# Kernel optimization log

Hardware: AMD Instinct MI355X
Metric: run time of the kernel (lower is better)

## Reference

```python
import jax, jax.numpy as jnp
import numpy as np

N = 50000
IN_F = 512
HID = 64
HEADS = 4
CLASSES = 6
E = 800000
NEG_SLOPE = 0.2


def setup_inputs() -> dict:
    key = jax.random.key(0)
    ks = jax.random.split(key, 12)
    s = 1.0 / np.sqrt(IN_F)
    s2 = 1.0 / np.sqrt(HID * HEADS)
    return {
        "x": jax.random.normal(ks[0], (N, IN_F), dtype=jnp.float32),
        "edge_index": jax.random.randint(ks[1], (2, E), 0, N, dtype=jnp.int32),
        "W1": jax.random.normal(ks[2], (IN_F, HEADS * HID), dtype=jnp.float32) * s,
        "a_src1": jax.random.normal(ks[3], (HEADS, HID), dtype=jnp.float32) * s,
        "a_dst1": jax.random.normal(ks[4], (HEADS, HID), dtype=jnp.float32) * s,
        "b1": jnp.zeros((HEADS * HID,), dtype=jnp.float32),
        "W2": jax.random.normal(ks[5], (HEADS * HID, CLASSES), dtype=jnp.float32) * s2,
        "a_src2": jax.random.normal(ks[6], (1, CLASSES), dtype=jnp.float32) * s2,
        "a_dst2": jax.random.normal(ks[7], (1, CLASSES), dtype=jnp.float32) * s2,
        "b2": jnp.zeros((CLASSES,), dtype=jnp.float32),
    }


def gat_conv(x, src, dst, W, a_src, a_dst, bias, heads, ch):
    # x: [N, F] -> h: [N, H, C]
    n = x.shape[0]
    h = (x @ W).reshape(n, heads, ch)
    # per-node attention halves: [N, H]
    e_src = jnp.einsum('nhc,hc->nh', h, a_src)
    e_dst = jnp.einsum('nhc,hc->nh', h, a_dst)
    # per-edge logits with leaky relu: [E', H]
    logits = jax.nn.leaky_relu(e_src[src] + e_dst[dst], NEG_SLOPE)
    # segment softmax over incoming edges of each dst node
    m = jax.ops.segment_max(logits, dst, num_segments=n)  # [N, H]
    p = jnp.exp(logits - m[dst])
    denom = jax.ops.segment_sum(p, dst, num_segments=n)   # [N, H] (>0: self loops)
    alpha = p / denom[dst]                                 # [E', H]
    # weighted scatter-aggregate: [N, H, C]
    out = jax.ops.segment_sum(alpha[:, :, None] * h[src], dst, num_segments=n)
    return out.reshape(n, heads * ch) + bias


def reference(x, edge_index, W1, a_src1, a_dst1, b1, W2, a_src2, a_dst2, b2):
    n = x.shape[0]
    loops = jnp.arange(n, dtype=edge_index.dtype)
    src = jnp.concatenate([edge_index[0], loops])  # PyG add_self_loops
    dst = jnp.concatenate([edge_index[1], loops])
    h = gat_conv(x, src, dst, W1, a_src1, a_dst1, b1, HEADS, HID)
    h = jax.nn.elu(h)
    out = gat_conv(h, src, dst, W2, a_src2, a_dst2, b2, 1, CLASSES)
    return jax.nn.log_softmax(out, axis=1)
```

## Files before the change

kernel.cpp:

```cpp
#include <hip/hip_runtime.h>

#define HEADS 4
#define HID 64
#define CH1 256
#define CLS 6
#define H2S 8
#define NSLOPE 0.2f

typedef short bf16x8 __attribute__((ext_vector_type(8)));
typedef float f32x4 __attribute__((ext_vector_type(4)));

__device__ __forceinline__ float leaky(float x) {
  return (x >= 0.f) ? x : NSLOPE * x;
}

__device__ __forceinline__ ushort f2bf(float f) {
  unsigned u = __float_as_uint(f);
  unsigned r = (u + 0x7FFFu + ((u >> 16) & 1u)) >> 16;
  return (ushort)r;
}

__device__ __forceinline__ float bf2f(ushort u) {
  return __uint_as_float((unsigned)u << 16);
}

__device__ __forceinline__ void gload16(const void* g, void* l) {
  __builtin_amdgcn_global_load_lds((const __attribute__((address_space(1))) void*)g,
                                   (__attribute__((address_space(3))) void*)l, 16, 0, 0);
}

__global__ void k_count_cvt_x(const int* __restrict__ ei, int E, int Etot,
                              int* __restrict__ cnt, int eb,
                              const float* __restrict__ W1, ushort* __restrict__ w1t,
                              const float* __restrict__ x, ushort* __restrict__ xb,
                              long nx) {
  int b = blockIdx.x;
  if (b < eb) {
    int e = b * 256 + threadIdx.x;
    if (e >= Etot) return;
    int d = (e < E) ? ei[E + e] : e - E;
    atomicAdd(&cnt[d], 1);
  } else if (b < eb + 512) {
    int t = (b - eb) * 256 + threadIdx.x;
    if (t >= 512 * 256) return;
    int k = t >> 8, c = t & 255;
    w1t[c * 512 + k] = f2bf(W1[t]);
  } else {
    long i = ((long)(b - eb - 512) * 256 + threadIdx.x) * 4;
    long stride = 2048L * 1024;
    for (; i + 3 < nx; i += stride) {
      float4 v = *(const float4*)&x[i];
      ushort4 o;
      o.x = f2bf(v.x); o.y = f2bf(v.y); o.z = f2bf(v.z); o.w = f2bf(v.w);
      *(ushort4*)&xb[i] = o;
    }
  }
}

__global__ __launch_bounds__(256) void k_gemm1_scatter(
    const ushort* __restrict__ xb,
    const ushort* __restrict__ w1t,
    const float* __restrict__ a_src, const float* __restrict__ a_dst,
    ushort* __restrict__ h1b, float* __restrict__ es, float* __restrict__ ed,
    int M, int G1,
    const int* __restrict__ ei, int E, int Etot,
    const int* __restrict__ rowptr, int* __restrict__ cursor,
    int* __restrict__ esrc) {
  __shared__ ushort lds[2][10240];
  int t = threadIdx.x;

  if (blockIdx.x >= G1) {
    int e = (blockIdx.x - G1) * 256 + t;
    if (e >= Etot) return;
    int s, d;
    if (e < E) { s = ei[e]; d = ei[E + e]; } else { s = d = e - E; }
    int pos = rowptr[d] + atomicAdd(&cursor[d], 1);
    esrc[pos] = s;
    return;
  }

  int wid = t >> 6, lane = t & 63;
  int brow = blockIdx.x * 64;

  int rA = t >> 2;
  int sA = (t & 3) ^ (rA & 3);
  int rowA = brow + rA; if (rowA >= M) rowA = M - 1;
  const ushort* srcA  = xb  + (size_t)rowA * 512 + sA * 8;
  int cB = t >> 2;
  int sB = (t & 3) ^ (cB & 3);
  const ushort* srcB0 = w1t + (size_t)cB * 512 + sB * 8;
  int dA = t * 8;
  int dB = 2048 + t * 8;

  int l15 = lane & 15, g = lane >> 4;
  int sw = ((g ^ (lane & 3)) << 3);
  int aoff[4], boff[4];
#pragma unroll
  for (int m = 0; m < 4; ++m) aoff[m] = (m * 16 + l15) * 32 + sw;
#pragma unroll
  for (int n = 0; n < 4; ++n) boff[n] = 2048 + (wid * 64 + n * 16 + l15) * 32 + sw;

  f32x4 acc[4][4] = {};

#define STAGE(buf, koff) do { \
    gload16(srcA + (koff),              &lds[buf][dA]); \
    gload16(srcB0 + (koff),             &lds[buf][dB]); \
    gload16(srcB0 +  64 * 512 + (koff), &lds[buf][dB + 2048]); \
    gload16(srcB0 + 128 * 512 + (koff), &lds[buf][dB + 4096]); \
    gload16(srcB0 + 192 * 512 + (koff), &lds[buf][dB + 6144]); \
  } while (0)

  STAGE(0, 0);
  __syncthreads();
  int cur = 0;
  for (int kt = 0; kt < 16; ++kt) {
    if (kt < 15) STAGE(cur ^ 1, (kt + 1) * 32);
    const ushort* L = lds[cur];
    bf16x8 av[4], bv[4];
#pragma unroll
    for (int m = 0; m < 4; ++m) av[m] = *(const bf16x8*)&L[aoff[m]];
#pragma unroll
    for (int n = 0; n < 4; ++n) bv[n] = *(const bf16x8*)&L[boff[n]];
#pragma unroll
    for (int m = 0; m < 4; ++m)
#pragma unroll
      for (int n = 0; n < 4; ++n)
        acc[m][n] = __builtin_amdgcn_mfma_f32_16x16x32_bf16(av[m], bv[n], acc[m][n], 0, 0, 0);
    __syncthreads();
    cur ^= 1;
  }
#undef STAGE

  float as4[4], ad4[4];
#pragma unroll
  for (int n = 0; n < 4; ++n) {
    int c = wid * 64 + n * 16 + l15;
    as4[n] = a_src[c];
    ad4[n] = a_dst[c];
  }
  int rbase = g * 4;
#pragma unroll
  for (int m = 0; m < 4; ++m) {
#pragma unroll
    for (int r = 0; r < 4; ++r) {
      int grow = brow + m * 16 + rbase + r;
      bool ok = grow < M;
      float ps = 0.f, pd = 0.f;
#pragma unroll
      for (int n = 0; n < 4; ++n) {
        float v = acc[m][n][r];
        ps += v * as4[n];
        pd += v * ad4[n];
        if (ok) h1b[(size_t)grow * CH1 + wid * 64 + n * 16 + l15] = f2bf(v);
      }
#pragma unroll
      for (int o = 1; o < 16; o <<= 1) {
        ps += __shfl_xor(ps, o);
        pd += __shfl_xor(pd, o);
      }
      if (l15 == 0 && ok) {
        es[grow * HEADS + wid] = ps;
        ed[grow * HEADS + wid] = pd;
      }
    }
  }
}

__global__ __launch_bounds__(256) void k_scan1(int* __restrict__ deg,
    int* __restrict__ rowptr, int* __restrict__ bsum, int n) {
  int i = blockIdx.x * 256 + threadIdx.x;
  int v = (i < n) ? deg[i] : 0;
  if (i < n) deg[i] = 0;
  int lane = threadIdx.x & 63, wave = threadIdx.x >> 6;
  int incl = v;
#pragma unroll
  for (int o = 1; o < 64; o <<= 1) {
    int u = __shfl_up(incl, o);
    if (lane >= o) incl += u;
  }
  __shared__ int ws4[4];
  if (lane == 63) ws4[wave] = incl;
  __syncthreads();
  if (threadIdx.x == 0) {
    int run = 0;
    for (int w = 0; w < 4; ++w) { int x = ws4[w]; ws4[w] = run; run += x; }
    bsum[blockIdx.x] = run;
  }
  __syncthreads();
  if (i < n) rowptr[i] = incl - v + ws4[wave];
}

__global__ __launch_bounds__(256) void k_scan3(int* __restrict__ rowptr,
    const int* __restrict__ bsum, int n, int Etot, int nb) {
  int t = threadIdx.x;
  int b = blockIdx.x;
  int v = (t < b && t < nb) ? bsum[t] : 0;
  int lane = t & 63, wave = t >> 6;
#pragma unroll
  for (int o = 32; o; o >>= 1) v += __shfl_xor(v, o);
  __shared__ int ws4[4];
  if (lane == 0) ws4[wave] = v;
  __syncthreads();
  int base = ws4[0] + ws4[1] + ws4[2] + ws4[3];
  int i = b * 256 + t;
  if (i < n) rowptr[i] += base;
  if (i == 0) rowptr[n] = Etot;
}

__global__ __launch_bounds__(256) void k_agg1_csr(const int* __restrict__ rowptr,
    const int* __restrict__ esrc, const float* __restrict__ es,
    const float* __restrict__ ed, const ushort* __restrict__ h1b,
    const float* __restrict__ b1, const float* __restrict__ W2,
    const float* __restrict__ a_src2, const float* __restrict__ a_dst2,
    float* __restrict__ h2, float* __restrict__ es2, float* __restrict__ ed2,
    int Nn) {
  __shared__ int   spi[4][64];
  __shared__ float spp[4][64 * 4];
  int wid = threadIdx.x >> 6, lane = threadIdx.x & 63;
  int ch = lane * 4;
  float w2s[4][CLS];
#pragma unroll
  for (int c = 0; c < 4; ++c)
#pragma unroll
    for (int j = 0; j < CLS; ++j)
      w2s[c][j] = W2[(ch + c) * CLS + j];

  int d = blockIdx.x * 4 + wid;
  if (d >= Nn) return;
  int beg = rowptr[d], end = rowptr[d + 1];
  float4 edv = *(const float4*)&ed[d * 4];
  int myhead = lane >> 4;
  const char* hcb = (const char*)h1b + (size_t)ch * 2;

  float4 acc = make_float4(0.f, 0.f, 0.f, 0.f);
  float4 den4 = make_float4(0.f, 0.f, 0.f, 0.f);
  const float* pp = &spp[wid][0];
  for (int c0 = beg; c0 < end; c0 += 64) {
    int i = c0 + lane;
    int s = 0;
    float4 p = make_float4(0.f, 0.f, 0.f, 0.f);
    if (i < end) {
      s = esrc[i];
      float4 e4 = *(const float4*)&es[s * 4];
      p.x = __expf(leaky(e4.x + edv.x));
      p.y = __expf(leaky(e4.y + edv.y));
      p.z = __expf(leaky(e4.z + edv.z));
      p.w = __expf(leaky(e4.w + edv.w));
    }
    den4.x += p.x; den4.y += p.y; den4.z += p.z; den4.w += p.w;
    spi[wid][lane] = s << 9;
    *(float4*)&spp[wid][lane * 4] = p;
    int cl = min(64, end - c0);
    int j = 0;
    for (; j + 3 < cl; j += 4) {
      int o0 = spi[wid][j],     o1 = spi[wid][j + 1];
      int o2 = spi[wid][j + 2], o3 = spi[wid][j + 3];
      float p0 = pp[j * 4 + myhead],       p1 = pp[(j + 1) * 4 + myhead];
      float p2 = pp[(j + 2) * 4 + myhead], p3 = pp[(j + 3) * 4 + myhead];
      ushort4 v0 = *(const ushort4*)(hcb + o0);
      ushort4 v1 = *(const ushort4*)(hcb + o1);
      ushort4 v2 = *(const ushort4*)(hcb + o2);
      ushort4 v3 = *(const ushort4*)(hcb + o3);
      acc.x += p0 * bf2f(v0.x) + p1 * bf2f(v1.x) + p2 * bf2f(v2.x) + p3 * bf2f(v3.x);
      acc.y += p0 * bf2f(v0.y) + p1 * bf2f(v1.y) + p2 * bf2f(v2.y) + p3 * bf2f(v3.y);
      acc.z += p0 * bf2f(v0.z) + p1 * bf2f(v1.z) + p2 * bf2f(v2.z) + p3 * bf2f(v3.z);
      acc.w += p0 * bf2f(v0.w) + p1 * bf2f(v1.w) + p2 * bf2f(v2.w) + p3 * bf2f(v3.w);
    }
    for (; j < cl; ++j) {
      int oj = spi[wid][j];
      float pj = pp[j * 4 + myhead];
      ushort4 v = *(const ushort4*)(hcb + oj);
      acc.x += pj * bf2f(v.x);
      acc.y += pj * bf2f(v.y);
      acc.z += pj * bf2f(v.z);
      acc.w += pj * bf2f(v.w);
    }
  }
#pragma unroll
  for (int o = 32; o; o >>= 1) {
    den4.x += __shfl_xor(den4.x, o);
    den4.y += __shfl_xor(den4.y, o);
    den4.z += __shfl_xor(den4.z, o);
    den4.w += __shfl_xor(den4.w, o);
  }
  float den = (myhead == 0) ? den4.x : (myhead == 1) ? den4.y
            : (myhead == 2) ? den4.z : den4.w;
  float4 b4 = *(const float4*)&b1[ch];
  float4 r;
  r.x = acc.x / den + b4.x; r.x = (r.x > 0.f) ? r.x : expm1f(r.x);
  r.y = acc.y / den + b4.y; r.y = (r.y > 0.f) ? r.y : expm1f(r.y);
  r.z = acc.z / den + b4.z; r.z = (r.z > 0.f) ? r.z : expm1f(r.z);
  r.w = acc.w / den + b4.w; r.w = (r.w > 0.f) ? r.w : expm1f(r.w);

  float q0 = r.x * w2s[0][0] + r.y * w2s[1][0] + r.z * w2s[2][0] + r.w * w2s[3][0];
  float q1 = r.x * w2s[0][1] + r.y * w2s[1][1] + r.z * w2s[2][1] + r.w * w2s[3][1];
  float q2 = r.x * w2s[0][2] + r.y * w2s[1][2] + r.z * w2s[2][2] + r.w * w2s[3][2];
  float q3 = r.x * w2s[0][3] + r.y * w2s[1][3] + r.z * w2s[2][3] + r.w * w2s[3][3];
  float q4 = r.x * w2s[0][4] + r.y * w2s[1][4] + r.z * w2s[2][4] + r.w * w2s[3][4];
  float q5 = r.x * w2s[0][5] + r.y * w2s[1][5] + r.z * w2s[2][5] + r.w * w2s[3][5];
#pragma unroll
  for (int o = 32; o; o >>= 1) {
    q0 += __shfl_xor(q0, o); q1 += __shfl_xor(q1, o); q2 += __shfl_xor(q2, o);
    q3 += __shfl_xor(q3, o); q4 += __shfl_xor(q4, o); q5 += __shfl_xor(q5, o);
  }
  if (lane == 0) {
    float* h2r = &h2[(size_t)d * H2S];
    h2r[0] = q0; h2r[1] = q1; h2r[2] = q2; h2r[3] = q3; h2r[4] = q4; h2r[5] = q5;
    es2[d] = q0 * a_src2[0] + q1 * a_src2[1] + q2 * a_src2[2]
           + q3 * a_src2[3] + q4 * a_src2[4] + q5 * a_src2[5];
    ed2[d] = q0 * a_dst2[0] + q1 * a_dst2[1] + q2 * a_dst2[2]
           + q3 * a_dst2[3] + q4 * a_dst2[4] + q5 * a_dst2[5];
  }
}

__global__ __launch_bounds__(256) void k_l2(const int* __restrict__ rowptr,
    const int* __restrict__ esrc, const float* __restrict__ es2,
    const float* __restrict__ ed2, const float* __restrict__ h2,
    const float* __restrict__ b2, float* __restrict__ out, int Nn) {
  int t = threadIdx.x;
  int grp = t >> 3, sl = t & 7;
  int n = blockIdx.x * 32 + grp;
  if (n >= Nn) return;
  int beg = rowptr[n], end = rowptr[n + 1];
  float edv = ed2[n];
  float den = 0.f, a0 = 0.f, a1 = 0.f, a2 = 0.f, a3 = 0.f, a4 = 0.f, a5 = 0.f;
  for (int i = beg + sl; i < end; i += 8) {
    int s = esrc[i];
    float p = __expf(leaky(es2[s] + edv));
    den += p;
    const float* hr = &h2[(size_t)s * H2S];
    float4 v0 = *(const float4*)hr;
    float2 v1 = *(const float2*)(hr + 4);
    a0 += p * v0.x; a1 += p * v0.y; a2 += p * v0.z;
    a3 += p * v0.w; a4 += p * v1.x; a5 += p * v1.y;
  }
#pragma unroll
  for (int o = 1; o < 8; o <<= 1) {
    den += __shfl_xor(den, o);
    a0 += __shfl_xor(a0, o); a1 += __shfl_xor(a1, o); a2 += __shfl_xor(a2, o);
    a3 += __shfl_xor(a3, o); a4 += __shfl_xor(a4, o); a5 += __shfl_xor(a5, o);
  }
  if (sl == 0) {
    float v[CLS];
    v[0] = a0 / den + b2[0]; v[1] = a1 / den + b2[1]; v[2] = a2 / den + b2[2];
    v[3] = a3 / den + b2[3]; v[4] = a4 / den + b2[4]; v[5] = a5 / den + b2[5];
    float mx = -1e30f;
#pragma unroll
    for (int j = 0; j < CLS; ++j) mx = fmaxf(mx, v[j]);
    float sum = 0.f;
#pragma unroll
    for (int j = 0; j < CLS; ++j) sum += __expf(v[j] - mx);
    float l = mx + logf(sum);
#pragma unroll
    for (int j = 0; j < CLS; ++j) out[n * CLS + j] = v[j] - l;
  }
}

extern "C" void kernel_launch(void* const* d_in, const int* in_sizes, int n_in,
                              void* d_out, int out_size, void* d_ws, size_t ws_size,
                              hipStream_t stream) {
  const float* x      = (const float*)d_in[0];
  const int*   ei     = (const int*)d_in[1];
  const float* W1     = (const float*)d_in[2];
  const float* a_src1 = (const float*)d_in[3];
  const float* a_dst1 = (const float*)d_in[4];
  const float* b1     = (const float*)d_in[5];
  const float* W2     = (const float*)d_in[6];
  const float* a_src2 = (const float*)d_in[7];
  const float* a_dst2 = (const float*)d_in[8];
  const float* b2     = (const float*)d_in[9];
  float* out = (float*)d_out;

  const int IN_F = 512;
  int N = in_sizes[0] / IN_F;
  int E = in_sizes[1] / 2;
  int Etot = E + N;

  float* ws = (float*)d_ws;
  size_t off = 0;
  ushort* xb  = (ushort*)(ws + off); off += (size_t)N * 256;
  ushort* h1b = (ushort*)(ws + off); off += (size_t)N * 128;
  float* es1  = ws + off; off += (size_t)N * HEADS;
  float* ed1  = ws + off; off += (size_t)N * HEADS;
  float* h2   = ws + off; off += (size_t)N * H2S;
  float* es2  = ws + off; off += (size_t)N;
  float* ed2  = ws + off; off += (size_t)N;
  int* rowptr = (int*)(ws + off); off += (size_t)N + 1;
  int* cursor = (int*)(ws + off); off += (size_t)N;
  int* bsum   = (int*)(ws + off); off += 256;
  int* esrc   = (int*)(ws + off); off += (size_t)Etot;
  ushort* w1t = (ushort*)(ws + off); off += (512 * 256 * 2 + 3) / 4;

  int nb = (N + 255) / 256;
  int eb = (Etot + 255) / 256;
  int G1 = (N + 63) / 64;

  hipMemsetAsync(cursor, 0, (size_t)N * 4, stream);
  k_count_cvt_x<<<eb + 512 + 2048, 256, 0, stream>>>(ei, E, Etot, cursor, eb,
                                                     W1, w1t, x, xb, (long)N * IN_F);
  k_scan1<<<nb, 256, 0, stream>>>(cursor, rowptr, bsum, N);
  k_scan3<<<nb, 256, 0, stream>>>(rowptr, bsum, N, Etot, nb);

  k_gemm1_scatter<<<G1 + eb, 256, 0, stream>>>(xb, w1t, a_src1, a_dst1,
                                               h1b, es1, ed1, N, G1,
                                               ei, E, Etot, rowptr, cursor, esrc);

  k_agg1_csr<<<(N + 3) / 4, 256, 0, stream>>>(rowptr, esrc, es1, ed1, h1b, b1,
                                              W2, a_src2, a_dst2, h2, es2, ed2, N);
  k_l2<<<(N + 31) / 32, 256, 0, stream>>>(rowptr, esrc, es2, ed2, h2, b2, out, N);
}
```

Measured before the change: 248.6 us.

## Split edge scatter from GEMM1 and shrink GEMM row tile to 32

Moves the CSR edge scatter out of the fused GEMM kernel into its own launch, and halves the GEMM1 row tile from 64 to 32 rows per block with separate A/B LDS buffers. The smaller tile doubles the number of GEMM blocks to raise occupancy and parallelism, and shrinks per-block LDS and accumulator registers. In exchange, every block reloads the full W1 tile, doubling weight traffic per row, and the extra kernel launch gives up the overlap between scatter and GEMM work.

```diff
diff --git a/kernel.cpp b/kernel.cpp
--- a/kernel.cpp
+++ b/kernel.cpp
@@ -57,57 +57,44 @@
   }
 }
 
-__global__ __launch_bounds__(256) void k_gemm1_scatter(
+__global__ __launch_bounds__(256) void k_gemm1_mfma(
     const ushort* __restrict__ xb,
     const ushort* __restrict__ w1t,
     const float* __restrict__ a_src, const float* __restrict__ a_dst,
     ushort* __restrict__ h1b, float* __restrict__ es, float* __restrict__ ed,
-    int M, int G1,
-    const int* __restrict__ ei, int E, int Etot,
-    const int* __restrict__ rowptr, int* __restrict__ cursor,
-    int* __restrict__ esrc) {
-  __shared__ ushort lds[2][10240];
+    int M) {
+  __shared__ ushort ldsA[2][1024];
+  __shared__ ushort ldsB[2][8192];
   int t = threadIdx.x;
-
-  if (blockIdx.x >= G1) {
-    int e = (blockIdx.x - G1) * 256 + t;
-    if (e >= Etot) return;
-    int s, d;
-    if (e < E) { s = ei[e]; d = ei[E + e]; } else { s = d = e - E; }
-    int pos = rowptr[d] + atomicAdd(&cursor[d], 1);
-    esrc[pos] = s;
-    return;
-  }
-
   int wid = t >> 6, lane = t & 63;
-  int brow = blockIdx.x * 64;
-
-  int rA = t >> 2;
-  int sA = (t & 3) ^ (rA & 3);
+  int brow = blockIdx.x * 32;
+
+  int rA = t >> 2, qA = t & 3, sA = qA ^ (rA & 3);
   int rowA = brow + rA; if (rowA >= M) rowA = M - 1;
-  const ushort* srcA  = xb  + (size_t)rowA * 512 + sA * 8;
+  const ushort* srcA = xb + (size_t)rowA * 512 + sA * 8;
+  int dA = t * 8;
+
   int cB = t >> 2;
   int sB = (t & 3) ^ (cB & 3);
   const ushort* srcB0 = w1t + (size_t)cB * 512 + sB * 8;
-  int dA = t * 8;
-  int dB = 2048 + t * 8;
+  int dB = t * 8;
 
   int l15 = lane & 15, g = lane >> 4;
   int sw = ((g ^ (lane & 3)) << 3);
-  int aoff[4], boff[4];
-#pragma unroll
-  for (int m = 0; m < 4; ++m) aoff[m] = (m * 16 + l15) * 32 + sw;
-#pragma unroll
-  for (int n = 0; n < 4; ++n) boff[n] = 2048 + (wid * 64 + n * 16 + l15) * 32 + sw;
-
-  f32x4 acc[4][4] = {};
+  int aoff[2], boff[4];
+#pragma unroll
+  for (int m = 0; m < 2; ++m) aoff[m] = (m * 16 + l15) * 32 + sw;
+#pragma unroll
+  for (int n = 0; n < 4; ++n) boff[n] = (wid * 64 + n * 16 + l15) * 32 + sw;
+
+  f32x4 acc[2][4] = {};
 
 #define STAGE(buf, koff) do { \
-    gload16(srcA + (koff),              &lds[buf][dA]); \
-    gload16(srcB0 + (koff),             &lds[buf][dB]); \
-    gload16(srcB0 +  64 * 512 + (koff), &lds[buf][dB + 2048]); \
-    gload16(srcB0 + 128 * 512 + (koff), &lds[buf][dB + 4096]); \
-    gload16(srcB0 + 192 * 512 + (koff), &lds[buf][dB + 6144]); \
+    if (t < 128) gload16(srcA + (koff), &ldsA[buf][dA]); \
+    gload16(srcB0 + (koff),             &ldsB[buf][dB]); \
+    gload16(srcB0 +  64 * 512 + (koff), &ldsB[buf][dB + 2048]); \
+    gload16(srcB0 + 128 * 512 + (koff), &ldsB[buf][dB + 4096]); \
+    gload16(srcB0 + 192 * 512 + (koff), &ldsB[buf][dB + 6144]); \
   } while (0)
 
   STAGE(0, 0);
@@ -115,14 +102,13 @@
   int cur = 0;
   for (int kt = 0; kt < 16; ++kt) {
     if (kt < 15) STAGE(cur ^ 1, (kt + 1) * 32);
-    const ushort* L = lds[cur];
-    bf16x8 av[4], bv[4];
-#pragma unroll
-    for (int m = 0; m < 4; ++m) av[m] = *(const bf16x8*)&L[aoff[m]];
-#pragma unroll
-    for (int n = 0; n < 4; ++n) bv[n] = *(const bf16x8*)&L[boff[n]];
-#pragma unroll
-    for (int m = 0; m < 4; ++m)
+    bf16x8 av[2], bv[4];
+#pragma unroll
+    for (int m = 0; m < 2; ++m) av[m] = *(const bf16x8*)&ldsA[cur][aoff[m]];
+#pragma unroll
+    for (int n = 0; n < 4; ++n) bv[n] = *(const bf16x8*)&ldsB[cur][boff[n]];
+#pragma unroll
+    for (int m = 0; m < 2; ++m)
 #pragma unroll
       for (int n = 0; n < 4; ++n)
         acc[m][n] = __builtin_amdgcn_mfma_f32_16x16x32_bf16(av[m], bv[n], acc[m][n], 0, 0, 0);
@@ -140,7 +126,7 @@
   }
   int rbase = g * 4;
 #pragma unroll
-  for (int m = 0; m < 4; ++m) {
+  for (int m = 0; m < 2; ++m) {
 #pragma unroll
     for (int r = 0; r < 4; ++r) {
       int grow = brow + m * 16 + rbase + r;
@@ -205,6 +191,17 @@
   int i = b * 256 + t;
   if (i < n) rowptr[i] += base;
   if (i == 0) rowptr[n] = Etot;
+}
+
+__global__ void k_scatter(const int* __restrict__ ei, int E, int Etot,
+    const int* __restrict__ rowptr, int* __restrict__ cursor,
+    int* __restrict__ esrc) {
+  int e = blockIdx.x * blockDim.x + threadIdx.x;
+  if (e >= Etot) return;
+  int s, d;
+  if (e < E) { s = ei[e]; d = ei[E + e]; } else { s = d = e - E; }
+  int pos = rowptr[d] + atomicAdd(&cursor[d], 1);
+  esrc[pos] = s;
 }
 
 __global__ __launch_bounds__(256) void k_agg1_csr(const int* __restrict__ rowptr,
@@ -393,19 +390,18 @@
 
   int nb = (N + 255) / 256;
   int eb = (Etot + 255) / 256;
-  int G1 = (N + 63) / 64;
 
   hipMemsetAsync(cursor, 0, (size_t)N * 4, stream);
   k_count_cvt_x<<<eb + 512 + 2048, 256, 0, stream>>>(ei, E, Etot, cursor, eb,
                                                      W1, w1t, x, xb, (long)N * IN_F);
   k_scan1<<<nb, 256, 0, stream>>>(cursor, rowptr, bsum, N);
   k_scan3<<<nb, 256, 0, stream>>>(rowptr, bsum, N, Etot, nb);
-
-  k_gemm1_scatter<<<G1 + eb, 256, 0, stream>>>(xb, w1t, a_src1, a_dst1,
-                                               h1b, es1, ed1, N, G1,
-                                               ei, E, Etot, rowptr, cursor, esrc);
-
+  k_scatter<<<eb, 256, 0, stream>>>(ei, E, Etot, rowptr, cursor, esrc);
+
+  k_gemm1_mfma<<<(N + 31) / 32, 256, 0, stream>>>(xb, w1t, a_src1, a_dst1,
+                                                  h1b, es1, ed1, N);
   k_agg1_csr<<<(N + 3) / 4, 256, 0, stream>>>(rowptr, esrc, es1, ed1, h1b, b1,
                                               W2, a_src2, a_dst2, h2, es2, ed2, N);
+
   k_l2<<<(N + 31) / 32, 256, 0, stream>>>(rowptr, esrc, es2, ed2, h2, b2, out, N);
 }
```

Result: slower. 260.4 us (+4.8%).
